# Kernel optimization log

Hardware: AMD Instinct MI355X
Metric: run time of the kernel (lower is better)

Reference implementation:

```python
import jax, jax.numpy as jnp
import numpy as np

UNITS = 128
N_CLASSES = 10
N_FEAT = 3
R_ON = 0.05      # time-gate open ratio
ALPHA = 0.001    # leak during closed phase
LN_EPS = 1e-3    # keras LayerNormalization default epsilon


def _time_gate(t, tau, s):
    # t: [B], tau/s: [U] -> k: [B, U]
    phi = jnp.mod(t[:, None] - s, tau) / tau
    k = jnp.where(phi < 0.5 * R_ON, 2.0 * phi / R_ON,
        jnp.where(phi < R_ON, 2.0 - 2.0 * phi / R_ON, ALPHA * phi))
    return k


def _plstm_step(x, t, h, c, Wx, Wh, b, tau, s):
    z = x @ Wx + h @ Wh + b                      # [B, 4U]
    i, f, g, o = jnp.split(z, 4, axis=-1)
    c_hat = jax.nn.sigmoid(f) * c + jax.nn.sigmoid(i) * jnp.tanh(g)
    h_hat = jax.nn.sigmoid(o) * jnp.tanh(c_hat)
    k = _time_gate(t, tau, s)
    return k * h_hat + (1.0 - k) * h, k * c_hat + (1.0 - k) * c


def _layer_norm(x, gamma, beta):
    mu = jnp.mean(x, axis=-1, keepdims=True)
    var = jnp.mean(jnp.square(x - mu), axis=-1, keepdims=True)
    return gamma * (x - mu) * jax.lax.rsqrt(var + LN_EPS) + beta


def setup_inputs() -> dict:
    key = jax.random.key(0)
    ks = jax.random.split(key, 16)
    B, T, F, U, C = 256, 1000, N_FEAT, UNITS, N_CLASSES
    inputs = jax.random.normal(ks[0], (B, T, F), dtype=jnp.float32)
    # strictly increasing-ish observation times per sequence
    times = jnp.cumsum(jax.random.uniform(ks[1], (B, T), dtype=jnp.float32), axis=1)
    sc_in = 1.0 / np.sqrt(F)
    sc_h = 1.0 / np.sqrt(U)
    Wx0 = jax.random.normal(ks[2], (F, 4 * U), dtype=jnp.float32) * sc_in
    Wh0 = jax.random.normal(ks[3], (U, 4 * U), dtype=jnp.float32) * sc_h
    b0 = jnp.zeros((4 * U,), dtype=jnp.float32)
    tau0 = jnp.exp(jax.random.uniform(ks[4], (U,), minval=0.0, maxval=3.0, dtype=jnp.float32))
    s0 = jax.random.uniform(ks[5], (U,), dtype=jnp.float32) * tau0
    Wx1 = jax.random.normal(ks[6], (U, 4 * U), dtype=jnp.float32) * sc_h
    Wh1 = jax.random.normal(ks[7], (U, 4 * U), dtype=jnp.float32) * sc_h
    b1 = jnp.zeros((4 * U,), dtype=jnp.float32)
    tau1 = jnp.exp(jax.random.uniform(ks[8], (U,), minval=0.0, maxval=3.0, dtype=jnp.float32))
    s1 = jax.random.uniform(ks[9], (U,), dtype=jnp.float32) * tau1
    gamma = jnp.ones((U,), dtype=jnp.float32)
    beta = jnp.zeros((U,), dtype=jnp.float32)
    Wfc = jax.random.normal(ks[10], (U, C), dtype=jnp.float32) * sc_h
    bfc = jnp.zeros((C,), dtype=jnp.float32)
    return {"inputs": inputs, "times": times, "Wx0": Wx0, "Wh0": Wh0, "b0": b0,
            "tau0": tau0, "s0": s0, "Wx1": Wx1, "Wh1": Wh1, "b1": b1,
            "tau1": tau1, "s1": s1, "gamma": gamma, "beta": beta,
            "Wfc": Wfc, "bfc": bfc}


def reference(inputs, times, Wx0, Wh0, b0, tau0, s0, Wx1, Wh1, b1, tau1, s1,
              gamma, beta, Wfc, bfc):
    B, T, F = inputs.shape
    U = Wh0.shape[0]
    x_t = jnp.transpose(inputs, (1, 0, 2))   # [T, B, F]
    t_t = jnp.transpose(times, (1, 0))       # [T, B]

    def step(carry, xt):
        h0, c0, h1, c1 = carry
        x, t = xt
        h0, c0 = _plstm_step(x, t, h0, c0, Wx0, Wh0, b0, tau0, s0)
        hn = _layer_norm(h0, gamma, beta)
        h1, c1 = _plstm_step(hn, t, h1, c1, Wx1, Wh1, b1, tau1, s1)
        probs = jax.nn.softmax(h1 @ Wfc + bfc, axis=-1)
        return (h0, c0, h1, c1), probs

    zeros = jnp.zeros((B, U), dtype=inputs.dtype)
    init = (zeros, zeros, zeros, zeros)
    _, out = jax.lax.scan(step, init, (x_t, t_t))  # out: [T, B, C]
    return jnp.transpose(out, (1, 0, 2))           # [B, T, C]
```

## Files before the change

kernel.cpp:

```cpp
#include <hip/hip_runtime.h>
#include <math.h>

constexpr int U      = 128;
constexpr int G4     = 512;
constexpr int NCls   = 10;
constexpr int TSTEPS = 1000;
constexpr int BATCH  = 256;


__device__ __forceinline__ float sigm(float x) {
    return 1.0f / (1.0f + __expf(-x));
}

__device__ __forceinline__ float tgate(float t, float tau, float s) {
    float r = fmodf(t - s, tau);
    if (r < 0.0f) r += tau;
    const float phi = r / tau;
    return (phi < 0.025f) ? 40.0f * phi
         : (phi < 0.05f)  ? 2.0f - 40.0f * phi
         : 0.001f * phi;
}

#define ROW4(WP, I, HB) { \
    float4 w_; \
    w_ = (WP)[((I)+0)*128]; ac.x += (HB).x*w_.x; ac.y += (HB).x*w_.y; ac.z += (HB).x*w_.z; ac.w += (HB).x*w_.w; \
    w_ = (WP)[((I)+1)*128]; ac.x += (HB).y*w_.x; ac.y += (HB).y*w_.y; ac.z += (HB).y*w_.z; ac.w += (HB).y*w_.w; \
    w_ = (WP)[((I)+2)*128]; ac.x += (HB).z*w_.x; ac.y += (HB).z*w_.y; ac.z += (HB).z*w_.z; ac.w += (HB).z*w_.w; \
    w_ = (WP)[((I)+3)*128]; ac.x += (HB).w*w_.x; ac.y += (HB).w*w_.y; ac.z += (HB).w*w_.z; ac.w += (HB).w*w_.w; }

#define ROW4P(W0, W1, W2, W3, HB) { \
    ac.x += (HB).x*(W0).x; ac.y += (HB).x*(W0).y; ac.z += (HB).x*(W0).z; ac.w += (HB).x*(W0).w; \
    ac.x += (HB).y*(W1).x; ac.y += (HB).y*(W1).y; ac.z += (HB).y*(W1).z; ac.w += (HB).y*(W1).w; \
    ac.x += (HB).z*(W2).x; ac.y += (HB).z*(W2).y; ac.z += (HB).z*(W2).z; ac.w += (HB).z*(W2).w; \
    ac.x += (HB).w*(W3).x; ac.y += (HB).w*(W3).y; ac.z += (HB).w*(W3).z; ac.w += (HB).w*(W3).w; }

__global__ __launch_bounds__(512, 1) void plstm_fused(
    const float* __restrict__ inputs,
    const float* __restrict__ times,
    const float* __restrict__ Wx0,
    const float* __restrict__ Wh0,
    const float* __restrict__ b0,
    const float* __restrict__ tau0,
    const float* __restrict__ s0,
    const float* __restrict__ Wx1,
    const float* __restrict__ Wh1,
    const float* __restrict__ b1,
    const float* __restrict__ tau1,
    const float* __restrict__ s1,
    const float* __restrict__ gamma_,
    const float* __restrict__ beta_,
    const float* __restrict__ Wfc,
    const float* __restrict__ bfc,
    float* __restrict__ out)
{
    const int tid = threadIdx.x;
    const int c4  = tid & 127;
    const int g   = tid >> 7;
    const int b   = blockIdx.x;

    __shared__ __align__(16) float wh0c[48 * G4];
    __shared__ __align__(16) float zuA[4 * G4];
    __shared__ __align__(16) float zuB[4 * G4];
    __shared__ __align__(16) float h0s[U];
    __shared__ __align__(16) float ghu[2 * U];
    __shared__ __align__(16) float b0s[G4], b1s[G4], Ps[G4], Qs[G4];
    __shared__ __align__(16) float wx0s[3 * G4];
    __shared__ __align__(16) float wfcs[U * 11];
    __shared__ float tau0s[U], s0s[U], tau1s[U], s1s[U];
    __shared__ float bfcs[NCls];
    __shared__ float red[4];
    __shared__ float gms[U], bts[U];

    if (tid < U) {
        gms[tid] = gamma_[tid]; bts[tid] = beta_[tid];
        tau0s[tid] = tau0[tid]; s0s[tid] = s0[tid];
        tau1s[tid] = tau1[tid]; s1s[tid] = s1[tid];
        h0s[tid] = 0.f; ghu[tid] = 0.f; ghu[U + tid] = 0.f;
    }
    {
        float4* dst = reinterpret_cast<float4*>(wh0c);
        #pragma unroll
        for (int i = 0; i < 12; ++i) {
            const int idx  = i * 512 + tid;
            const int slot = idx >> 7;
            const int cq   = idx & 127;
            const int grp  = slot / 12;
            const int row  = 32 * grp + 12 + (slot - grp * 12);
            dst[slot * 128 + cq] =
                *reinterpret_cast<const float4*>(&Wh0[row * G4 + 4 * cq]);
        }
    }
    if (tid < G4) { b0s[tid] = b0[tid]; b1s[tid] = b1[tid]; }
    for (int i = tid; i < 3 * G4; i += 512) wx0s[i] = Wx0[i];
    for (int i = tid; i < U * NCls; i += 512) {
        const int u = i / NCls, c = i - u * NCls;
        wfcs[u * 11 + c] = Wfc[i];
    }
    if (tid < NCls) bfcs[tid] = bfc[tid];
    __syncthreads();

    {
        float P = 0.f, Q = 0.f;
        #pragma unroll 8
        for (int u = 0; u < U; ++u) {
            const float w = Wx1[u * G4 + tid];
            Q += gms[u] * w;
            P += bts[u] * w;
        }
        Ps[tid] = P; Qs[tid] = Q;
    }

    float4 wh0r[12];
    #pragma unroll
    for (int i = 0; i < 12; ++i)
        wh0r[i] = *reinterpret_cast<const float4*>(&Wh0[(32 * g + i) * G4 + 4 * c4]);
    const float* __restrict__ Wc = (g < 2) ? Wx1 : Wh1;
    const int rb = 64 * (g & 1);
    float4 wcr[4];
    #pragma unroll
    for (int i = 0; i < 4; ++i)
        wcr[i] = *reinterpret_cast<const float4*>(&Wc[(rb + i) * G4 + 4 * c4]);

    float c0r = 0.f, h0r = 0.f, c1r = 0.f, h1r = 0.f;

    const float4* __restrict__ wlA =
        reinterpret_cast<const float4*>(wh0c) + (12 * g) * 128 + c4;
    const float4* __restrict__ wsA =
        reinterpret_cast<const float4*>(Wh0) + (32 * g + 24) * 128 + c4;
    const float4* __restrict__ wsC =
        reinterpret_cast<const float4*>(Wc) + (rb + 4) * 128 + c4;
    const float* __restrict__ hvC = ghu + 64 * g;

    const float* __restrict__ xp = inputs + (size_t)b * TSTEPS * 3;
    const float* __restrict__ tp = times  + (size_t)b * TSTEPS;
    float*       __restrict__ op = out    + (size_t)b * TSTEPS * NCls;

    float xa0 = xp[0], xa1 = xp[1], xa2 = xp[2], tva = tp[0];

    __syncthreads();

    for (int t = 0; t < TSTEPS; ++t) {
        const float x0 = xa0, x1 = xa1, x2 = xa2, tv = tva;
        const int tn = (t + 1 < TSTEPS) ? t + 1 : t;
        xa0 = xp[tn*3+0]; xa1 = xp[tn*3+1]; xa2 = xp[tn*3+2]; tva = tp[tn];

        {
            float4 ac = make_float4(0.f, 0.f, 0.f, 0.f);
            {
                const float4 hb0 = *reinterpret_cast<const float4*>(&h0s[32 * g + 0]);
                ROW4P(wh0r[0], wh0r[1], wh0r[2], wh0r[3], hb0);
                const float4 hb1 = *reinterpret_cast<const float4*>(&h0s[32 * g + 4]);
                ROW4P(wh0r[4], wh0r[5], wh0r[6], wh0r[7], hb1);
                const float4 hb2 = *reinterpret_cast<const float4*>(&h0s[32 * g + 8]);
                ROW4P(wh0r[8], wh0r[9], wh0r[10], wh0r[11], hb2);
            }
            #pragma unroll
            for (int i = 0; i < 12; i += 4) {
                const float4 hb = *reinterpret_cast<const float4*>(&h0s[32 * g + 12 + i]);
                ROW4(wlA, i, hb);
            }
            #pragma unroll
            for (int i = 0; i < 8; i += 4) {
                const float4 hb = *reinterpret_cast<const float4*>(&h0s[32 * g + 24 + i]);
                ROW4(wsA, i, hb);
            }
            *reinterpret_cast<float4*>(&zuA[g * G4 + 4 * c4]) = ac;
        }
        __syncthreads();

        if (tid < U) {
            const int u = tid;
            float z[4];
            #pragma unroll
            for (int q = 0; q < 4; ++q) {
                const int c = u + q * 128;
                float s = b0s[c] + x0 * wx0s[c] + x1 * wx0s[G4 + c] + x2 * wx0s[2 * G4 + c];
                s += (zuA[c] + zuA[G4 + c]) + (zuA[2 * G4 + c] + zuA[3 * G4 + c]);
                z[q] = s;
            }
            const float ig = sigm(z[0]), fg = sigm(z[1]);
            const float gg = tanhf(z[2]), og = sigm(z[3]);
            const float ch = fg * c0r + ig * gg;
            const float hh = og * tanhf(ch);
            const float k  = tgate(tv, tau0s[u], s0s[u]);
            const float hn = k * hh + (1.0f - k) * h0r;
            c0r = k * ch + (1.0f - k) * c0r;
            h0r = hn;
            h0s[u] = hn;
            ghu[u] = gms[u] * hn;
            float ssum = hn, qsum = hn * hn;
            #pragma unroll
            for (int off = 1; off < 64; off <<= 1) {
                ssum += __shfl_xor(ssum, off);
                qsum += __shfl_xor(qsum, off);
            }
            if ((tid & 63) == 0) {
                red[(tid >> 6) * 2]     = ssum;
                red[(tid >> 6) * 2 + 1] = qsum;
            }
        }
        __syncthreads();

        {
            float4 ac = make_float4(0.f, 0.f, 0.f, 0.f);
            {
                const float4 hb = *reinterpret_cast<const float4*>(&hvC[0]);
                ROW4P(wcr[0], wcr[1], wcr[2], wcr[3], hb);
            }
            #pragma unroll 5
            for (int i = 0; i < 60; i += 4) {
                const float4 hb = *reinterpret_cast<const float4*>(&hvC[4 + i]);
                ROW4(wsC, i, hb);
            }
            *reinterpret_cast<float4*>(&zuB[g * G4 + 4 * c4]) = ac;
        }
        __syncthreads();

        if (tid < U) {
            const float mu    = (red[0] + red[2]) * (1.0f / 128.0f);
            const float msq   = (red[1] + red[3]) * (1.0f / 128.0f);
            const float rstd  = rsqrtf(msq - mu * mu + 1e-3f);
            const float murstd = mu * rstd;
            const int u = tid;
            float z[4];
            #pragma unroll
            for (int q = 0; q < 4; ++q) {
                const int c = u + q * 128;
                const float sx = zuB[c] + zuB[G4 + c];
                const float sh = zuB[2 * G4 + c] + zuB[3 * G4 + c];
                z[q] = b1s[c] + Ps[c] + rstd * sx - murstd * Qs[c] + sh;
            }
            const float ig = sigm(z[0]), fg = sigm(z[1]);
            const float gg = tanhf(z[2]), og = sigm(z[3]);
            const float ch = fg * c1r + ig * gg;
            const float hh = og * tanhf(ch);
            const float k  = tgate(tv, tau1s[u], s1s[u]);
            const float hn = k * hh + (1.0f - k) * h1r;
            c1r = k * ch + (1.0f - k) * c1r;
            h1r = hn;
            ghu[U + u] = hn;
        }
        __syncthreads();

        if (tid < 64) {
            const float a  = ghu[U + tid];
            const float bv = ghu[U + tid + 64];
            float p[NCls];
            #pragma unroll
            for (int c = 0; c < NCls; ++c)
                p[c] = a * wfcs[tid * 11 + c] + bv * wfcs[(tid + 64) * 11 + c];
            #pragma unroll
            for (int off = 1; off < 64; off <<= 1) {
                #pragma unroll
                for (int c = 0; c < NCls; ++c) p[c] += __shfl_xor(p[c], off);
            }
            float m = -1e30f;
            #pragma unroll
            for (int c = 0; c < NCls; ++c) { p[c] += bfcs[c]; m = fmaxf(m, p[c]); }
            float ssum = 0.0f;
            #pragma unroll
            for (int c = 0; c < NCls; ++c) { p[c] = __expf(p[c] - m); ssum += p[c]; }
            const float inv = 1.0f / ssum;
            float pv = p[0];
            #pragma unroll
            for (int c = 1; c < NCls; ++c) if (tid == c) pv = p[c];
            if (tid < NCls) op[t * NCls + tid] = pv * inv;
        }
    }
}

extern "C" void kernel_launch(void* const* d_in, const int* in_sizes, int n_in,
                              void* d_out, int out_size, void* d_ws, size_t ws_size,
                              hipStream_t stream) {
    const float* inputs = (const float*)d_in[0];
    const float* times  = (const float*)d_in[1];
    const float* Wx0    = (const float*)d_in[2];
    const float* Wh0    = (const float*)d_in[3];
    const float* b0     = (const float*)d_in[4];
    const float* tau0   = (const float*)d_in[5];
    const float* s0     = (const float*)d_in[6];
    const float* Wx1    = (const float*)d_in[7];
    const float* Wh1    = (const float*)d_in[8];
    const float* b1     = (const float*)d_in[9];
    const float* tau1   = (const float*)d_in[10];
    const float* s1     = (const float*)d_in[11];
    const float* gamma_ = (const float*)d_in[12];
    const float* beta_  = (const float*)d_in[13];
    const float* Wfc    = (const float*)d_in[14];
    const float* bfc    = (const float*)d_in[15];
    float* out = (float*)d_out;

    dim3 grid(BATCH);
    dim3 block(512);
    hipLaunchKernelGGL(plstm_fused, grid, block, 0, stream,
                       inputs, times, Wx0, Wh0, b0, tau0, s0,
                       Wx1, Wh1, b1, tau1, s1, gamma_, beta_, Wfc, bfc, out);
}
```

Before: 6.842 ms.

## Overlap layer-1 Wh1 matvec with LN and merge cell update with softmax in one wave

Waves 2-3 (the Wh1·h1 part) now start their recurrent matvec before the barrier that follows layer-0's update, since they do not depend on the new h0. Waves 0-1 do the Wx1·LN(h0) part after that barrier. The layer-1 cell update and the FC/softmax are merged into a single wave (wave 2) that handles two units per lane, which removes one __syncthreads per timestep. The cost is a serialized 2-unit update on one wave instead of 128 threads in parallel, and any ordering hazard on ghu/h1 reads across waves.

```diff
diff --git a/kernel.cpp b/kernel.cpp
--- a/kernel.cpp
+++ b/kernel.cpp
@@ -121,7 +121,8 @@
     for (int i = 0; i < 4; ++i)
         wcr[i] = *reinterpret_cast<const float4*>(&Wc[(rb + i) * G4 + 4 * c4]);
 
-    float c0r = 0.f, h0r = 0.f, c1r = 0.f, h1r = 0.f;
+    float c0r = 0.f, h0r = 0.f;
+    float c1A = 0.f, h1A = 0.f, c1B = 0.f, h1B = 0.f;
 
     const float4* __restrict__ wlA =
         reinterpret_cast<const float4*>(wh0c) + (12 * g) * 128 + c4;
@@ -199,9 +200,7 @@
                 red[(tid >> 6) * 2 + 1] = qsum;
             }
         }
-        __syncthreads();
-
-        {
+        if (g >= 2) {
             float4 ac = make_float4(0.f, 0.f, 0.f, 0.f);
             {
                 const float4 hb = *reinterpret_cast<const float4*>(&hvC[0]);
@@ -216,39 +215,56 @@
         }
         __syncthreads();
 
-        if (tid < U) {
+        if (g < 2) {
+            float4 ac = make_float4(0.f, 0.f, 0.f, 0.f);
+            {
+                const float4 hb = *reinterpret_cast<const float4*>(&hvC[0]);
+                ROW4P(wcr[0], wcr[1], wcr[2], wcr[3], hb);
+            }
+            #pragma unroll 5
+            for (int i = 0; i < 60; i += 4) {
+                const float4 hb = *reinterpret_cast<const float4*>(&hvC[4 + i]);
+                ROW4(wsC, i, hb);
+            }
+            *reinterpret_cast<float4*>(&zuB[g * G4 + 4 * c4]) = ac;
+        }
+        __syncthreads();
+
+        if ((tid >> 6) == 2) {
+            const int lane = tid & 63;
             const float mu    = (red[0] + red[2]) * (1.0f / 128.0f);
             const float msq   = (red[1] + red[3]) * (1.0f / 128.0f);
             const float rstd  = rsqrtf(msq - mu * mu + 1e-3f);
             const float murstd = mu * rstd;
-            const int u = tid;
-            float z[4];
-            #pragma unroll
-            for (int q = 0; q < 4; ++q) {
-                const int c = u + q * 128;
-                const float sx = zuB[c] + zuB[G4 + c];
-                const float sh = zuB[2 * G4 + c] + zuB[3 * G4 + c];
-                z[q] = b1s[c] + Ps[c] + rstd * sx - murstd * Qs[c] + sh;
-            }
-            const float ig = sigm(z[0]), fg = sigm(z[1]);
-            const float gg = tanhf(z[2]), og = sigm(z[3]);
-            const float ch = fg * c1r + ig * gg;
-            const float hh = og * tanhf(ch);
-            const float k  = tgate(tv, tau1s[u], s1s[u]);
-            const float hn = k * hh + (1.0f - k) * h1r;
-            c1r = k * ch + (1.0f - k) * c1r;
-            h1r = hn;
-            ghu[U + u] = hn;
-        }
-        __syncthreads();
-
-        if (tid < 64) {
-            const float a  = ghu[U + tid];
-            const float bv = ghu[U + tid + 64];
+            float hnv[2];
+            #pragma unroll
+            for (int e = 0; e < 2; ++e) {
+                const int u = lane + e * 64;
+                float z[4];
+                #pragma unroll
+                for (int q = 0; q < 4; ++q) {
+                    const int c = u + q * 128;
+                    const float sx = zuB[c] + zuB[G4 + c];
+                    const float sh = zuB[2 * G4 + c] + zuB[3 * G4 + c];
+                    z[q] = b1s[c] + Ps[c] + rstd * sx - murstd * Qs[c] + sh;
+                }
+                const float ig = sigm(z[0]), fg = sigm(z[1]);
+                const float gg = tanhf(z[2]), og = sigm(z[3]);
+                const float cprev = e ? c1B : c1A;
+                const float hprev = e ? h1B : h1A;
+                const float ch = fg * cprev + ig * gg;
+                const float hh = og * tanhf(ch);
+                const float k  = tgate(tv, tau1s[u], s1s[u]);
+                const float hn = k * hh + (1.0f - k) * hprev;
+                if (e) { c1B = k * ch + (1.0f - k) * c1B; h1B = hn; }
+                else   { c1A = k * ch + (1.0f - k) * c1A; h1A = hn; }
+                ghu[U + u] = hn;
+                hnv[e] = hn;
+            }
             float p[NCls];
             #pragma unroll
             for (int c = 0; c < NCls; ++c)
-                p[c] = a * wfcs[tid * 11 + c] + bv * wfcs[(tid + 64) * 11 + c];
+                p[c] = hnv[0] * wfcs[lane * 11 + c] + hnv[1] * wfcs[(lane + 64) * 11 + c];
             #pragma unroll
             for (int off = 1; off < 64; off <<= 1) {
                 #pragma unroll
@@ -263,8 +279,8 @@
             const float inv = 1.0f / ssum;
             float pv = p[0];
             #pragma unroll
-            for (int c = 1; c < NCls; ++c) if (tid == c) pv = p[c];
-            if (tid < NCls) op[t * NCls + tid] = pv * inv;
+            for (int c = 1; c < NCls; ++c) if (lane == c) pv = p[c];
+            if (lane < NCls) op[t * NCls + lane] = pv * inv;
         }
     }
 }
```

New measurement: 11.44 ms. 1.67x slower.
